# Performance work log

Hardware: AMD Instinct MI355X
Metric: run time of the kernel (lower is better)

The kernel has to match this reference:

```python
import jax, jax.numpy as jnp
import numpy as np

N_NODES = 100000
N_EDGES = 1600000
IN_DIM = 128      # 1 (degree) + 127 (raw feat)
HID = 128
N_GRAPHS = 100


def setup_inputs() -> dict:
    key = jax.random.key(0)
    ks = jax.random.split(key, 16)
    feat = jax.random.normal(ks[0], (N_NODES, IN_DIM - 1), dtype=jnp.float32)
    src = jax.random.randint(ks[1], (N_EDGES,), 0, N_NODES, dtype=jnp.int32)
    dst = jax.random.randint(ks[2], (N_EDGES,), 0, N_NODES, dtype=jnp.int32)
    graph_ids = jnp.sort(jax.random.randint(ks[3], (N_NODES,), 0, N_GRAPHS, dtype=jnp.int32))
    s = 1.0 / np.sqrt(IN_DIM)
    W0 = jax.random.uniform(ks[4], (HID, IN_DIM), jnp.float32, -s, s)
    b0 = jax.random.uniform(ks[5], (HID,), jnp.float32, -s, s)
    s = 1.0 / np.sqrt(HID)
    W1 = jax.random.uniform(ks[6], (HID, HID), jnp.float32, -s, s)
    b1 = jax.random.uniform(ks[7], (HID,), jnp.float32, -s, s)
    W2 = jax.random.uniform(ks[8], (HID, HID), jnp.float32, -s, s)
    b2 = jax.random.uniform(ks[9], (HID,), jnp.float32, -s, s)
    Wc1 = jax.random.uniform(ks[10], (HID, HID), jnp.float32, -s, s)
    bc1 = jax.random.uniform(ks[11], (HID,), jnp.float32, -s, s)
    Wc2 = jax.random.uniform(ks[12], (1, HID), jnp.float32, -s, s)
    bc2 = jax.random.uniform(ks[13], (1,), jnp.float32, -s, s)
    return {"feat": feat, "src": src, "dst": dst, "graph_ids": graph_ids,
            "num_graphs": N_GRAPHS,
            "W0": W0, "b0": b0, "W1": W1, "b1": b1, "W2": W2, "b2": b2,
            "Wc1": Wc1, "bc1": bc1, "Wc2": Wc2, "bc2": bc2}


def _gcn_layer(h, src, dst, deg, W, b):
    # mean over in-neighbor messages; zero-in-degree nodes keep old h (DGL reduce never fires)
    n = h.shape[0]
    summed = jax.ops.segment_sum(h[src], dst, num_segments=n)  # [N, d]
    mean = summed / jnp.maximum(deg, 1.0)[:, None]
    agg = jnp.where((deg > 0)[:, None], mean, h)
    return jax.nn.relu(agg @ W.T + b)


def reference(feat, src, dst, graph_ids, num_graphs,
              W0, b0, W1, b1, W2, b2, Wc1, bc1, Wc2, bc2):
    n = feat.shape[0]
    deg = jax.ops.segment_sum(jnp.ones(src.shape[0], jnp.float32), dst, num_segments=n)  # in-degrees
    h = jnp.concatenate([deg[:, None], feat], axis=-1)  # [N, IN_DIM]
    for W, b in ((W0, b0), (W1, b1), (W2, b2)):
        h = _gcn_layer(h, src, dst, deg, W, b)
    # dgl.mean_nodes: per-graph mean of node features
    counts = jax.ops.segment_sum(jnp.ones(n, jnp.float32), graph_ids, num_segments=num_graphs)
    hg = jax.ops.segment_sum(h, graph_ids, num_segments=num_graphs) / jnp.maximum(counts, 1.0)[:, None]
    # faithful: classify1 applied twice, no activation (F.relu was passed as bias flag)
    hg = hg @ Wc1.T + bc1
    hg = hg @ Wc1.T + bc1
    hg = hg @ Wc2.T + bc2
    return hg  # [num_graphs, 1]
```

## Files before the change

### kernel.cpp

```cpp
#include <hip/hip_runtime.h>
#include <hip/hip_bf16.h>

#define HID 128
#define NRAW 127
#define BSH 8
#define BNODES 256


typedef __attribute__((ext_vector_type(8))) short short8;
typedef __attribute__((ext_vector_type(4))) float floatx4;
typedef __attribute__((ext_vector_type(2))) float floatx2;

__device__ inline unsigned pack_bf2(float x, float y) {
    unsigned bx = __float_as_uint(x);
    unsigned by = __float_as_uint(y);
    bx += 0x7fffu + ((bx >> 16) & 1u);
    by += 0x7fffu + ((by >> 16) & 1u);
    return (bx >> 16) | (by & 0xffff0000u);
}
__device__ inline float bf_lo(unsigned u) { return __uint_as_float(u << 16); }
__device__ inline float bf_hi(unsigned u) { return __uint_as_float(u & 0xffff0000u); }


__global__ void init_kernel(const float* __restrict__ W0, const float* __restrict__ W1,
                            const float* __restrict__ W2, const float* __restrict__ Wc1,
                            unsigned* __restrict__ O0, unsigned* __restrict__ O1,
                            unsigned* __restrict__ O2, float* __restrict__ Wc1p,
                            int* __restrict__ gbucket, float* __restrict__ hg,
                            float* __restrict__ counts, int G) {
    int id = blockIdx.x * blockDim.x + threadIdx.x;
    if (id < 512) gbucket[id] = 0;
    if (id < G * HID) hg[id] = 0.f;
    if (id < G) counts[id] = 0.f;
    if (id < 16384) {
        int t = id >> 7, p = id & 127;
        Wc1p[id] = Wc1[t * 128 + ((p & 7) * 16 + (p >> 3))];
    }
    if (id < 3 * 8192) {
        int sel = id >> 13, l = id & 8191;
        const float* W = sel == 0 ? W0 : (sel == 1 ? W1 : W2);
        unsigned* O = sel == 0 ? O0 : (sel == 1 ? O1 : O2);
        int o = l >> 6, pp = (l & 63) * 2;
        int k0 = (pp & 7) * 16 + (pp >> 3);
        int k1 = ((pp + 1) & 7) * 16 + ((pp + 1) >> 3);
        O[l] = pack_bf2(W[o * 128 + k0], W[o * 128 + k1]);
    }
}


__global__ __launch_bounds__(256) void bucket_count_kernel(const int* __restrict__ dst,
                                                           int* __restrict__ gbucket,
                                                           int E, int NB) {
    __shared__ int hist[512];
    int t = threadIdx.x;
    for (int b = t; b < NB; b += 256) hist[b] = 0;
    __syncthreads();
    int base = blockIdx.x * 4096;
    #pragma unroll
    for (int j = 0; j < 16; ++j) {
        int e = base + j * 256 + t;
        if (e < E) atomicAdd(&hist[dst[e] >> BSH], 1);
    }
    __syncthreads();
    for (int b = t; b < NB; b += 256) {
        int v = hist[b];
        if (v) atomicAdd(&gbucket[b], v);
    }
}

__global__ void bucket_scan_kernel(const int* __restrict__ gbucket, int* __restrict__ bstart,
                                   int* __restrict__ gcur, int NB, int E) {
    __shared__ int sm[512];
    int t = threadIdx.x;
    int v = (t < NB) ? gbucket[t] : 0;
    sm[t] = v;
    __syncthreads();
    for (int off = 1; off < 512; off <<= 1) {
        int add = (t >= off) ? sm[t - off] : 0;
        __syncthreads();
        sm[t] += add;
        __syncthreads();
    }
    if (t < NB) {
        int ex = sm[t] - v;
        bstart[t] = ex;
        gcur[t] = ex;
    }
    if (t == 0) bstart[NB] = E;
}

__global__ __launch_bounds__(256) void bucket_scatter_kernel(const int* __restrict__ src,
                                                             const int* __restrict__ dst,
                                                             int* __restrict__ gcur,
                                                             uint2* __restrict__ staging,
                                                             int E, int NB) {
    __shared__ int hist[512];
    __shared__ int base[512];
    int t = threadIdx.x;
    for (int b = t; b < NB; b += 256) hist[b] = 0;
    __syncthreads();
    int s[16], d[16], r[16];
    int e0 = blockIdx.x * 4096;
    #pragma unroll
    for (int j = 0; j < 16; ++j) {
        int e = e0 + j * 256 + t;
        if (e < E) {
            s[j] = src[e];
            d[j] = dst[e];
            r[j] = atomicAdd(&hist[d[j] >> BSH], 1);
        } else d[j] = -1;
    }
    __syncthreads();
    for (int b = t; b < NB; b += 256) {
        int v = hist[b];
        base[b] = v ? atomicAdd(&gcur[b], v) : 0;
    }
    __syncthreads();
    #pragma unroll
    for (int j = 0; j < 16; ++j) {
        if (d[j] >= 0) {
            int b = d[j] >> BSH;
            staging[base[b] + r[j]] = make_uint2((unsigned)s[j], (unsigned)d[j]);
        }
    }
}

__global__ __launch_bounds__(256) void csr_build_kernel(const uint2* __restrict__ staging,
                                                        const int* __restrict__ bstart,
                                                        int* __restrict__ rp, int* __restrict__ csr,
                                                        float* __restrict__ degf,
                                                        int N, int E, int NB) {
    __shared__ int hist[256];
    __shared__ int sm[256];
    __shared__ int excl[256];
    __shared__ int cnt[256];
    int t = threadIdx.x;
    int b = blockIdx.x;
    int nbase = b << BSH;
    int s0 = bstart[b], e1 = bstart[b + 1];
    hist[t] = 0;
    __syncthreads();
    for (int i = s0 + t; i < e1; i += 256) {
        uint2 p = staging[i];
        atomicAdd(&hist[p.y & (BNODES - 1)], 1);
    }
    __syncthreads();
    int h = hist[t];
    sm[t] = h;
    __syncthreads();
    for (int off = 1; off < 256; off <<= 1) {
        int add = (t >= off) ? sm[t - off] : 0;
        __syncthreads();
        sm[t] += add;
        __syncthreads();
    }
    excl[t] = sm[t] - h;
    cnt[t] = 0;
    int n = nbase + t;
    if (n < N) {
        rp[n] = s0 + (sm[t] - h);
        degf[n] = (float)h;
    }
    if (b == NB - 1 && t == 0) rp[N] = E;
    __syncthreads();
    for (int i = s0 + t; i < e1; i += 256) {
        uint2 p = staging[i];
        int dl = p.y & (BNODES - 1);
        int pos = s0 + excl[dl] + atomicAdd(&cnt[dl], 1);
        csr[pos] = (int)p.x;
    }
}


__global__ void build_h0_kernel(const float* __restrict__ feat,
                                unsigned* __restrict__ h8, int N) {
    int id = blockIdx.x * blockDim.x + threadIdx.x;
    if (id >= N * 32) return;
    int n = id >> 5, c = id & 31;
    const float* fr = feat + (size_t)n * NRAW;
    int base = c >> 1, hb = (c & 1) * 4;
    float f[4];
    #pragma unroll
    for (int j = 0; j < 4; ++j) {
        int l = (hb + j) * 16 + base;
        f[j] = (l == 0) ? 0.f : fr[l - 1];
    }
    unsigned w = __builtin_amdgcn_cvt_pk_fp8_f32(f[0], f[1], 0, false);
    w = __builtin_amdgcn_cvt_pk_fp8_f32(f[2], f[3], w, true);
    h8[id] = w;
}


__global__ __launch_bounds__(256) void agg_fp8_kernel(const unsigned* __restrict__ h8,
                                                      unsigned* __restrict__ agg,
                                                      const int* __restrict__ rp,
                                                      const int* __restrict__ csr,
                                                      const float* __restrict__ degf, int N) {
    int t = threadIdx.x;
    int col = t & 15;
    int i = blockIdx.x * 16 + (t >> 4);
    if (i >= N) return;
    int start = rp[i], end = rp[i + 1];
    int deg = end - start;
    const uint2* h2 = (const uint2*)h8;
    if (deg == 0) {
        uint2 v = h2[(size_t)i * 16 + col];
        floatx2 l0 = __builtin_amdgcn_cvt_pk_f32_fp8(v.x, false);
        floatx2 h0 = __builtin_amdgcn_cvt_pk_f32_fp8(v.x, true);
        floatx2 l1 = __builtin_amdgcn_cvt_pk_f32_fp8(v.y, false);
        floatx2 h1 = __builtin_amdgcn_cvt_pk_f32_fp8(v.y, true);
        uint4 r;
        r.x = pack_bf2(l0[0], l0[1]);
        r.y = pack_bf2(h0[0], h0[1]);
        r.z = pack_bf2(l1[0], l1[1]);
        r.w = pack_bf2(h1[0], h1[1]);
        ((uint4*)agg)[(size_t)i * 16 + col] = r;
        return;
    }
    floatx2 a0 = {0.f, 0.f}, a1 = {0.f, 0.f}, a2 = {0.f, 0.f}, a3 = {0.f, 0.f};
    float dsum = 0.f;
    int p = start;
    for (; p + 4 <= end; p += 4) {
        int i0 = csr[p];
        int i1 = csr[p + 1];
        int i2 = csr[p + 2];
        int i3 = csr[p + 3];
        uint2 v0 = h2[(size_t)i0 * 16 + col];
        uint2 v1 = h2[(size_t)i1 * 16 + col];
        uint2 v2 = h2[(size_t)i2 * 16 + col];
        uint2 v3 = h2[(size_t)i3 * 16 + col];
        if (degf && col == 0) dsum += degf[i0] + degf[i1] + degf[i2] + degf[i3];
        a0 += __builtin_amdgcn_cvt_pk_f32_fp8(v0.x, false);
        a1 += __builtin_amdgcn_cvt_pk_f32_fp8(v0.x, true);
        a2 += __builtin_amdgcn_cvt_pk_f32_fp8(v0.y, false);
        a3 += __builtin_amdgcn_cvt_pk_f32_fp8(v0.y, true);
        a0 += __builtin_amdgcn_cvt_pk_f32_fp8(v1.x, false);
        a1 += __builtin_amdgcn_cvt_pk_f32_fp8(v1.x, true);
        a2 += __builtin_amdgcn_cvt_pk_f32_fp8(v1.y, false);
        a3 += __builtin_amdgcn_cvt_pk_f32_fp8(v1.y, true);
        a0 += __builtin_amdgcn_cvt_pk_f32_fp8(v2.x, false);
        a1 += __builtin_amdgcn_cvt_pk_f32_fp8(v2.x, true);
        a2 += __builtin_amdgcn_cvt_pk_f32_fp8(v2.y, false);
        a3 += __builtin_amdgcn_cvt_pk_f32_fp8(v2.y, true);
        a0 += __builtin_amdgcn_cvt_pk_f32_fp8(v3.x, false);
        a1 += __builtin_amdgcn_cvt_pk_f32_fp8(v3.x, true);
        a2 += __builtin_amdgcn_cvt_pk_f32_fp8(v3.y, false);
        a3 += __builtin_amdgcn_cvt_pk_f32_fp8(v3.y, true);
    }
    for (; p < end; ++p) {
        int i0 = csr[p];
        uint2 v0 = h2[(size_t)i0 * 16 + col];
        if (degf && col == 0) dsum += degf[i0];
        a0 += __builtin_amdgcn_cvt_pk_f32_fp8(v0.x, false);
        a1 += __builtin_amdgcn_cvt_pk_f32_fp8(v0.x, true);
        a2 += __builtin_amdgcn_cvt_pk_f32_fp8(v0.y, false);
        a3 += __builtin_amdgcn_cvt_pk_f32_fp8(v0.y, true);
    }
    if (degf && col == 0) a0[0] = dsum;
    float inv = 1.f / (float)deg;
    uint4 r;
    r.x = pack_bf2(a0[0] * inv, a0[1] * inv);
    r.y = pack_bf2(a1[0] * inv, a1[1] * inv);
    r.z = pack_bf2(a2[0] * inv, a2[1] * inv);
    r.w = pack_bf2(a3[0] * inv, a3[1] * inv);
    ((uint4*)agg)[(size_t)i * 16 + col] = r;
}


__global__ __launch_bounds__(256) void mfma_gemm_kernel(const unsigned* __restrict__ A,
                                                        unsigned* __restrict__ out8,
                                                        unsigned* __restrict__ outb,
                                                        const unsigned* __restrict__ Wb,
                                                        const float* __restrict__ bias, int N) {
    int t = threadIdx.x;
    int wv = t >> 6, lane = t & 63;
    int m = lane & 15, q = lane >> 4;
    int n0 = blockIdx.x * 64;
    const unsigned* abase = A + (size_t)(n0 + wv * 16 + m) * 64 + q * 4;

    floatx4 acc[8];
    #pragma unroll
    for (int ot = 0; ot < 8; ++ot) acc[ot] = (floatx4)(0.f);

    #pragma unroll
    for (int kt = 0; kt < 4; ++kt) {
        short8 af = *(const short8*)(abase + kt * 16);
        short8 bf[8];
        #pragma unroll
        for (int ot = 0; ot < 8; ++ot)
            bf[ot] = *(const short8*)&Wb[(ot * 16 + m) * 64 + kt * 16 + q * 4];
        #pragma unroll
        for (int ot = 0; ot < 8; ++ot)
            acc[ot] = __builtin_amdgcn_mfma_f32_16x16x32_bf16(af, bf[ot], acc[ot], 0, 0, 0);
    }

    float bv[8];
    #pragma unroll
    for (int ot = 0; ot < 8; ++ot) bv[ot] = bias[ot * 16 + m];

    #pragma unroll
    for (int r = 0; r < 4; ++r) {
        int n = n0 + wv * 16 + q * 4 + r;
        if (n < N) {
            float vv[8];
            #pragma unroll
            for (int ot = 0; ot < 8; ++ot) vv[ot] = fmaxf(acc[ot][r] + bv[ot], 0.f);
            if (out8) {
                unsigned w0 = __builtin_amdgcn_cvt_pk_fp8_f32(vv[0], vv[1], 0, false);
                w0 = __builtin_amdgcn_cvt_pk_fp8_f32(vv[2], vv[3], w0, true);
                unsigned w1 = __builtin_amdgcn_cvt_pk_fp8_f32(vv[4], vv[5], 0, false);
                w1 = __builtin_amdgcn_cvt_pk_fp8_f32(vv[6], vv[7], w1, true);
                ((uint2*)out8)[(size_t)n * 16 + m] = make_uint2(w0, w1);
            }
            if (outb) {
                uint4 w;
                w.x = pack_bf2(vv[0], vv[1]);
                w.y = pack_bf2(vv[2], vv[3]);
                w.z = pack_bf2(vv[4], vv[5]);
                w.w = pack_bf2(vv[6], vv[7]);
                ((uint4*)outb)[(size_t)n * 16 + m] = w;
            }
        }
    }
}


__global__ __launch_bounds__(256) void pool_kernel(const unsigned* __restrict__ h,
                                                   const int* __restrict__ gid,
                                                   float* __restrict__ hg,
                                                   float* __restrict__ counts, int N) {
    int c = threadIdx.x & 63;
    int q = threadIdx.x >> 6;
    int n0 = blockIdx.x * 64;
    int nend = min(n0 + 64, N);
    float ax = 0.f, ay = 0.f, cnt = 0.f;
    int cur = -1;
    for (int n = n0 + q; n < nend; n += 4) {
        int g = gid[n];
        if (g != cur) {
            if (cur >= 0) {
                atomicAdd(&hg[cur * HID + 2 * c], ax);
                atomicAdd(&hg[cur * HID + 2 * c + 1], ay);
                if (c == 0) atomicAdd(&counts[cur], cnt);
            }
            ax = ay = cnt = 0.f;
            cur = g;
        }
        unsigned v = h[(size_t)n * 64 + c];
        ax += bf_lo(v); ay += bf_hi(v);
        cnt += 1.f;
    }
    if (cur >= 0) {
        atomicAdd(&hg[cur * HID + 2 * c], ax);
        atomicAdd(&hg[cur * HID + 2 * c + 1], ay);
        if (c == 0) atomicAdd(&counts[cur], cnt);
    }
}


__global__ __launch_bounds__(128) void cls_fused_kernel(const float* __restrict__ hg,
                                                        const float* __restrict__ counts,
                                                        const float* __restrict__ Wc1p,
                                                        const float* __restrict__ Wc1,
                                                        const float* __restrict__ bc1,
                                                        const float* __restrict__ Wc2,
                                                        const float* __restrict__ bc2,
                                                        float* __restrict__ out, int G) {
    __shared__ float x[128];
    __shared__ float y[128];
    __shared__ float red[128];
    int g = blockIdx.x, t = threadIdx.x;
    float inv = 1.f / fmaxf(counts[g], 1.f);
    x[t] = hg[g * HID + t] * inv;
    __syncthreads();
    const float4* wp4 = (const float4*)(Wc1p + t * HID);
    float s = 0.f;
    #pragma unroll
    for (int k4 = 0; k4 < 32; ++k4) {
        float4 w = wp4[k4];
        s += x[k4 * 4] * w.x + x[k4 * 4 + 1] * w.y + x[k4 * 4 + 2] * w.z + x[k4 * 4 + 3] * w.w;
    }
    y[t] = s + bc1[t];
    __syncthreads();
    const float4* w4 = (const float4*)(Wc1 + t * HID);
    float s2 = 0.f;
    #pragma unroll
    for (int k4 = 0; k4 < 32; ++k4) {
        float4 w = w4[k4];
        s2 += y[k4 * 4] * w.x + y[k4 * 4 + 1] * w.y + y[k4 * 4 + 2] * w.z + y[k4 * 4 + 3] * w.w;
    }
    red[t] = (s2 + bc1[t]) * Wc2[t];
    __syncthreads();
    if (t < 64) {
        float r = red[t] + red[t + 64];
        #pragma unroll
        for (int off = 32; off > 0; off >>= 1) r += __shfl_down(r, off);
        if (t == 0) out[g] = r + bc2[0];
    }
}


extern "C" void kernel_launch(void* const* d_in, const int* in_sizes, int n_in,
                              void* d_out, int out_size, void* d_ws, size_t ws_size,
                              hipStream_t stream) {
    const float* feat = (const float*)d_in[0];
    const int* src    = (const int*)d_in[1];
    const int* dst    = (const int*)d_in[2];
    const int* gid    = (const int*)d_in[3];
    const float* W0  = (const float*)d_in[5];
    const float* b0  = (const float*)d_in[6];
    const float* W1  = (const float*)d_in[7];
    const float* b1  = (const float*)d_in[8];
    const float* W2  = (const float*)d_in[9];
    const float* b2  = (const float*)d_in[10];
    const float* Wc1 = (const float*)d_in[11];
    const float* bc1 = (const float*)d_in[12];
    const float* Wc2 = (const float*)d_in[13];
    const float* bc2 = (const float*)d_in[14];

    const int N = in_sizes[3];
    const int E = in_sizes[1];
    const int G = out_size;
    const int NB = (N + BNODES - 1) >> BSH;

    char* ws = (char*)d_ws;
    size_t off = 0;
    auto alloc = [&](size_t bytes) { void* p = ws + off; off += (bytes + 255) & ~size_t(255); return p; };
    unsigned* h8     = (unsigned*)alloc((size_t)N * 32 * 4);
    unsigned* hB     = (unsigned*)alloc((size_t)N * 64 * 4);
    unsigned* aggbuf = (unsigned*)alloc((size_t)N * 64 * 4);
    float* degf      = (float*)alloc((size_t)N * 4);
    uint2* staging   = (uint2*)alloc((size_t)E * 8);
    int* csr         = (int*)alloc((size_t)E * 4);
    int* rp          = (int*)alloc((size_t)(N + 1) * 4);
    int* gbucket     = (int*)alloc(512 * 4);
    int* bstart      = (int*)alloc(513 * 4);
    int* gcur        = (int*)alloc(512 * 4);
    unsigned* Wb0    = (unsigned*)alloc(8192 * 4);
    unsigned* Wb1    = (unsigned*)alloc(8192 * 4);
    unsigned* Wb2    = (unsigned*)alloc(8192 * 4);
    float* Wc1p      = (float*)alloc(16384 * 4);
    float* hg        = (float*)alloc((size_t)G * HID * 4);
    float* counts    = (float*)alloc((size_t)G * 4);

    init_kernel<<<96, 256, 0, stream>>>(W0, W1, W2, Wc1, Wb0, Wb1, Wb2, Wc1p,
                                        gbucket, hg, counts, G);

    int gE = (E + 4095) / 4096;
    bucket_count_kernel<<<gE, 256, 0, stream>>>(dst, gbucket, E, NB);
    bucket_scan_kernel<<<1, 512, 0, stream>>>(gbucket, bstart, gcur, NB, E);
    bucket_scatter_kernel<<<gE, 256, 0, stream>>>(src, dst, gcur, staging, E, NB);
    csr_build_kernel<<<NB, 256, 0, stream>>>(staging, bstart, rp, csr, degf, N, E, NB);

    build_h0_kernel<<<(N * 32 + 255) / 256, 256, 0, stream>>>(feat, h8, N);

    int agg_grid = (N + 15) / 16;
    int gemm_grid = (N + 63) / 64;

    agg_fp8_kernel<<<agg_grid, 256, 0, stream>>>(h8, aggbuf, rp, csr, degf, N);
    mfma_gemm_kernel<<<gemm_grid, 256, 0, stream>>>(aggbuf, h8, nullptr, Wb0, b0, N);

    agg_fp8_kernel<<<agg_grid, 256, 0, stream>>>(h8, aggbuf, rp, csr, nullptr, N);
    mfma_gemm_kernel<<<gemm_grid, 256, 0, stream>>>(aggbuf, h8, nullptr, Wb1, b1, N);

    agg_fp8_kernel<<<agg_grid, 256, 0, stream>>>(h8, aggbuf, rp, csr, nullptr, N);
    mfma_gemm_kernel<<<gemm_grid, 256, 0, stream>>>(aggbuf, nullptr, hB, Wb2, b2, N);

    pool_kernel<<<(N + 63) / 64, 256, 0, stream>>>(hB, gid, hg, counts, N);

    cls_fused_kernel<<<G, 128, 0, stream>>>(hg, counts, Wc1p, Wc1, bc1, Wc2, bc2,
                                            (float*)d_out, G);
}
```

Before: 426.9 us.

## Fuse neighbor aggregation and MFMA GEMM into one kernel per GCN layer

Each GCN layer becomes one kernel. It gathers and averages the fp8 neighbor features of 16 nodes into LDS as bf16, runs the 16x128x128 MFMA GEMM from LDS, then stages the outputs in LDS for coalesced global writes. This drops the bf16 aggregation buffer's global write and reread and three kernel launches. Because the old kernels read and wrote the same h8 buffer in turn, it also ping-pongs between two fp8 buffers so a layer never overwrites features it is still gathering. The cost is that each block now reloads the full weight matrix for only 16 nodes, and the LDS barriers may make the gather and GEMM phases wait on each other.

```diff
diff --git a/kernel.cpp b/kernel.cpp
--- a/kernel.cpp
+++ b/kernel.cpp
@@ -191,135 +191,124 @@
 }
 
 
-__global__ __launch_bounds__(256) void agg_fp8_kernel(const unsigned* __restrict__ h8,
-                                                      unsigned* __restrict__ agg,
-                                                      const int* __restrict__ rp,
-                                                      const int* __restrict__ csr,
-                                                      const float* __restrict__ degf, int N) {
-    int t = threadIdx.x;
-    int col = t & 15;
-    int i = blockIdx.x * 16 + (t >> 4);
-    if (i >= N) return;
-    int start = rp[i], end = rp[i + 1];
-    int deg = end - start;
-    const uint2* h2 = (const uint2*)h8;
-    if (deg == 0) {
-        uint2 v = h2[(size_t)i * 16 + col];
-        floatx2 l0 = __builtin_amdgcn_cvt_pk_f32_fp8(v.x, false);
-        floatx2 h0 = __builtin_amdgcn_cvt_pk_f32_fp8(v.x, true);
-        floatx2 l1 = __builtin_amdgcn_cvt_pk_f32_fp8(v.y, false);
-        floatx2 h1 = __builtin_amdgcn_cvt_pk_f32_fp8(v.y, true);
-        uint4 r;
-        r.x = pack_bf2(l0[0], l0[1]);
-        r.y = pack_bf2(h0[0], h0[1]);
-        r.z = pack_bf2(l1[0], l1[1]);
-        r.w = pack_bf2(h1[0], h1[1]);
-        ((uint4*)agg)[(size_t)i * 16 + col] = r;
-        return;
-    }
-    floatx2 a0 = {0.f, 0.f}, a1 = {0.f, 0.f}, a2 = {0.f, 0.f}, a3 = {0.f, 0.f};
-    float dsum = 0.f;
-    int p = start;
-    for (; p + 4 <= end; p += 4) {
-        int i0 = csr[p];
-        int i1 = csr[p + 1];
-        int i2 = csr[p + 2];
-        int i3 = csr[p + 3];
-        uint2 v0 = h2[(size_t)i0 * 16 + col];
-        uint2 v1 = h2[(size_t)i1 * 16 + col];
-        uint2 v2 = h2[(size_t)i2 * 16 + col];
-        uint2 v3 = h2[(size_t)i3 * 16 + col];
-        if (degf && col == 0) dsum += degf[i0] + degf[i1] + degf[i2] + degf[i3];
-        a0 += __builtin_amdgcn_cvt_pk_f32_fp8(v0.x, false);
-        a1 += __builtin_amdgcn_cvt_pk_f32_fp8(v0.x, true);
-        a2 += __builtin_amdgcn_cvt_pk_f32_fp8(v0.y, false);
-        a3 += __builtin_amdgcn_cvt_pk_f32_fp8(v0.y, true);
-        a0 += __builtin_amdgcn_cvt_pk_f32_fp8(v1.x, false);
-        a1 += __builtin_amdgcn_cvt_pk_f32_fp8(v1.x, true);
-        a2 += __builtin_amdgcn_cvt_pk_f32_fp8(v1.y, false);
-        a3 += __builtin_amdgcn_cvt_pk_f32_fp8(v1.y, true);
-        a0 += __builtin_amdgcn_cvt_pk_f32_fp8(v2.x, false);
-        a1 += __builtin_amdgcn_cvt_pk_f32_fp8(v2.x, true);
-        a2 += __builtin_amdgcn_cvt_pk_f32_fp8(v2.y, false);
-        a3 += __builtin_amdgcn_cvt_pk_f32_fp8(v2.y, true);
-        a0 += __builtin_amdgcn_cvt_pk_f32_fp8(v3.x, false);
-        a1 += __builtin_amdgcn_cvt_pk_f32_fp8(v3.x, true);
-        a2 += __builtin_amdgcn_cvt_pk_f32_fp8(v3.y, false);
-        a3 += __builtin_amdgcn_cvt_pk_f32_fp8(v3.y, true);
-    }
-    for (; p < end; ++p) {
-        int i0 = csr[p];
-        uint2 v0 = h2[(size_t)i0 * 16 + col];
-        if (degf && col == 0) dsum += degf[i0];
-        a0 += __builtin_amdgcn_cvt_pk_f32_fp8(v0.x, false);
-        a1 += __builtin_amdgcn_cvt_pk_f32_fp8(v0.x, true);
-        a2 += __builtin_amdgcn_cvt_pk_f32_fp8(v0.y, false);
-        a3 += __builtin_amdgcn_cvt_pk_f32_fp8(v0.y, true);
-    }
-    if (degf && col == 0) a0[0] = dsum;
-    float inv = 1.f / (float)deg;
-    uint4 r;
-    r.x = pack_bf2(a0[0] * inv, a0[1] * inv);
-    r.y = pack_bf2(a1[0] * inv, a1[1] * inv);
-    r.z = pack_bf2(a2[0] * inv, a2[1] * inv);
-    r.w = pack_bf2(a3[0] * inv, a3[1] * inv);
-    ((uint4*)agg)[(size_t)i * 16 + col] = r;
-}
-
-
-__global__ __launch_bounds__(256) void mfma_gemm_kernel(const unsigned* __restrict__ A,
+__global__ __launch_bounds__(256) void gcn_fused_kernel(const unsigned* __restrict__ h8,
                                                         unsigned* __restrict__ out8,
                                                         unsigned* __restrict__ outb,
                                                         const unsigned* __restrict__ Wb,
-                                                        const float* __restrict__ bias, int N) {
+                                                        const float* __restrict__ bias,
+                                                        const int* __restrict__ rp,
+                                                        const int* __restrict__ csr,
+                                                        const float* __restrict__ degf, int N) {
+    __shared__ unsigned Al[16 * 64];
+    __shared__ unsigned Cs[16 * 64];
     int t = threadIdx.x;
+    int col = t & 15;
+    int g = t >> 4;
+    int n0 = blockIdx.x * 16;
+    int i = n0 + g;
+    const uint2* h2 = (const uint2*)h8;
+
+    if (i < N) {
+        int start = rp[i], end = rp[i + 1];
+        int deg = end - start;
+        uint4 r;
+        if (deg == 0) {
+            uint2 v = h2[(size_t)i * 16 + col];
+            floatx2 l0 = __builtin_amdgcn_cvt_pk_f32_fp8(v.x, false);
+            floatx2 h0 = __builtin_amdgcn_cvt_pk_f32_fp8(v.x, true);
+            floatx2 l1 = __builtin_amdgcn_cvt_pk_f32_fp8(v.y, false);
+            floatx2 h1 = __builtin_amdgcn_cvt_pk_f32_fp8(v.y, true);
+            r.x = pack_bf2(l0[0], l0[1]);
+            r.y = pack_bf2(h0[0], h0[1]);
+            r.z = pack_bf2(l1[0], l1[1]);
+            r.w = pack_bf2(h1[0], h1[1]);
+        } else {
+            floatx2 a0 = {0.f, 0.f}, a1 = {0.f, 0.f}, a2 = {0.f, 0.f}, a3 = {0.f, 0.f};
+            float dsum = 0.f;
+            int p = start;
+            for (; p + 4 <= end; p += 4) {
+                int i0 = csr[p];
+                int i1 = csr[p + 1];
+                int i2 = csr[p + 2];
+                int i3 = csr[p + 3];
+                uint2 v0 = h2[(size_t)i0 * 16 + col];
+                uint2 v1 = h2[(size_t)i1 * 16 + col];
+                uint2 v2 = h2[(size_t)i2 * 16 + col];
+                uint2 v3 = h2[(size_t)i3 * 16 + col];
+                if (degf && col == 0) dsum += degf[i0] + degf[i1] + degf[i2] + degf[i3];
+                a0 += __builtin_amdgcn_cvt_pk_f32_fp8(v0.x, false);
+                a1 += __builtin_amdgcn_cvt_pk_f32_fp8(v0.x, true);
+                a2 += __builtin_amdgcn_cvt_pk_f32_fp8(v0.y, false);
+                a3 += __builtin_amdgcn_cvt_pk_f32_fp8(v0.y, true);
+                a0 += __builtin_amdgcn_cvt_pk_f32_fp8(v1.x, false);
+                a1 += __builtin_amdgcn_cvt_pk_f32_fp8(v1.x, true);
+                a2 += __builtin_amdgcn_cvt_pk_f32_fp8(v1.y, false);
+                a3 += __builtin_amdgcn_cvt_pk_f32_fp8(v1.y, true);
+                a0 += __builtin_amdgcn_cvt_pk_f32_fp8(v2.x, false);
+                a1 += __builtin_amdgcn_cvt_pk_f32_fp8(v2.x, true);
+                a2 += __builtin_amdgcn_cvt_pk_f32_fp8(v2.y, false);
+                a3 += __builtin_amdgcn_cvt_pk_f32_fp8(v2.y, true);
+                a0 += __builtin_amdgcn_cvt_pk_f32_fp8(v3.x, false);
+                a1 += __builtin_amdgcn_cvt_pk_f32_fp8(v3.x, true);
+                a2 += __builtin_amdgcn_cvt_pk_f32_fp8(v3.y, false);
+                a3 += __builtin_amdgcn_cvt_pk_f32_fp8(v3.y, true);
+            }
+            for (; p < end; ++p) {
+                int i0 = csr[p];
+                uint2 v0 = h2[(size_t)i0 * 16 + col];
+                if (degf && col == 0) dsum += degf[i0];
+                a0 += __builtin_amdgcn_cvt_pk_f32_fp8(v0.x, false);
+                a1 += __builtin_amdgcn_cvt_pk_f32_fp8(v0.x, true);
+                a2 += __builtin_amdgcn_cvt_pk_f32_fp8(v0.y, false);
+                a3 += __builtin_amdgcn_cvt_pk_f32_fp8(v0.y, true);
+            }
+            if (degf && col == 0) a0[0] = dsum;
+            float inv = 1.f / (float)deg;
+            r.x = pack_bf2(a0[0] * inv, a0[1] * inv);
+            r.y = pack_bf2(a1[0] * inv, a1[1] * inv);
+            r.z = pack_bf2(a2[0] * inv, a2[1] * inv);
+            r.w = pack_bf2(a3[0] * inv, a3[1] * inv);
+        }
+        *(uint4*)&Al[(g * 16 + col) * 4] = r;
+    }
+    __syncthreads();
+
     int wv = t >> 6, lane = t & 63;
     int m = lane & 15, q = lane >> 4;
-    int n0 = blockIdx.x * 64;
-    const unsigned* abase = A + (size_t)(n0 + wv * 16 + m) * 64 + q * 4;
-
-    floatx4 acc[8];
-    #pragma unroll
-    for (int ot = 0; ot < 8; ++ot) acc[ot] = (floatx4)(0.f);
-
+    floatx4 acc0 = (floatx4)(0.f), acc1 = (floatx4)(0.f);
     #pragma unroll
     for (int kt = 0; kt < 4; ++kt) {
-        short8 af = *(const short8*)(abase + kt * 16);
-        short8 bf[8];
-        #pragma unroll
-        for (int ot = 0; ot < 8; ++ot)
-            bf[ot] = *(const short8*)&Wb[(ot * 16 + m) * 64 + kt * 16 + q * 4];
-        #pragma unroll
-        for (int ot = 0; ot < 8; ++ot)
-            acc[ot] = __builtin_amdgcn_mfma_f32_16x16x32_bf16(af, bf[ot], acc[ot], 0, 0, 0);
-    }
-
-    float bv[8];
-    #pragma unroll
-    for (int ot = 0; ot < 8; ++ot) bv[ot] = bias[ot * 16 + m];
-
-    #pragma unroll
-    for (int r = 0; r < 4; ++r) {
-        int n = n0 + wv * 16 + q * 4 + r;
+        short8 af = *(const short8*)&Al[m * 64 + (kt * 4 + q) * 4];
+        short8 b0 = *(const short8*)&Wb[((2 * wv) * 16 + m) * 64 + kt * 16 + q * 4];
+        short8 b1 = *(const short8*)&Wb[((2 * wv + 1) * 16 + m) * 64 + kt * 16 + q * 4];
+        acc0 = __builtin_amdgcn_mfma_f32_16x16x32_bf16(af, b0, acc0, 0, 0, 0);
+        acc1 = __builtin_amdgcn_mfma_f32_16x16x32_bf16(af, b1, acc1, 0, 0, 0);
+    }
+    float bv0 = bias[(2 * wv) * 16 + m];
+    float bv1 = bias[(2 * wv + 1) * 16 + m];
+    #pragma unroll
+    for (int r4 = 0; r4 < 4; ++r4) {
+        int row = q * 4 + r4;
+        float v0 = fmaxf(acc0[r4] + bv0, 0.f);
+        float v1 = fmaxf(acc1[r4] + bv1, 0.f);
+        if (out8) {
+            unsigned pk = __builtin_amdgcn_cvt_pk_fp8_f32(v0, v1, 0, false);
+            *(unsigned short*)((char*)Cs + row * 128 + m * 8 + 2 * wv) = (unsigned short)pk;
+        } else {
+            Cs[row * 64 + m * 4 + wv] = pack_bf2(v0, v1);
+        }
+    }
+    __syncthreads();
+
+    {
+        int row = t >> 4, c = t & 15;
+        int n = n0 + row;
         if (n < N) {
-            float vv[8];
-            #pragma unroll
-            for (int ot = 0; ot < 8; ++ot) vv[ot] = fmaxf(acc[ot][r] + bv[ot], 0.f);
-            if (out8) {
-                unsigned w0 = __builtin_amdgcn_cvt_pk_fp8_f32(vv[0], vv[1], 0, false);
-                w0 = __builtin_amdgcn_cvt_pk_fp8_f32(vv[2], vv[3], w0, true);
-                unsigned w1 = __builtin_amdgcn_cvt_pk_fp8_f32(vv[4], vv[5], 0, false);
-                w1 = __builtin_amdgcn_cvt_pk_fp8_f32(vv[6], vv[7], w1, true);
-                ((uint2*)out8)[(size_t)n * 16 + m] = make_uint2(w0, w1);
-            }
-            if (outb) {
-                uint4 w;
-                w.x = pack_bf2(vv[0], vv[1]);
-                w.y = pack_bf2(vv[2], vv[3]);
-                w.z = pack_bf2(vv[4], vv[5]);
-                w.w = pack_bf2(vv[6], vv[7]);
-                ((uint4*)outb)[(size_t)n * 16 + m] = w;
-            }
+            if (out8)
+                ((uint2*)out8)[(size_t)n * 16 + c] =
+                    *(const uint2*)((const char*)Cs + row * 128 + c * 8);
+            else
+                ((uint4*)outb)[(size_t)n * 16 + c] = *(const uint4*)&Cs[row * 64 + c * 4];
         }
     }
 }
@@ -426,9 +415,9 @@
     char* ws = (char*)d_ws;
     size_t off = 0;
     auto alloc = [&](size_t bytes) { void* p = ws + off; off += (bytes + 255) & ~size_t(255); return p; };
-    unsigned* h8     = (unsigned*)alloc((size_t)N * 32 * 4);
+    unsigned* h8a    = (unsigned*)alloc((size_t)N * 32 * 4);
+    unsigned* h8b    = (unsigned*)alloc((size_t)N * 32 * 4);
     unsigned* hB     = (unsigned*)alloc((size_t)N * 64 * 4);
-    unsigned* aggbuf = (unsigned*)alloc((size_t)N * 64 * 4);
     float* degf      = (float*)alloc((size_t)N * 4);
     uint2* staging   = (uint2*)alloc((size_t)E * 8);
     int* csr         = (int*)alloc((size_t)E * 4);
@@ -452,19 +441,12 @@
     bucket_scatter_kernel<<<gE, 256, 0, stream>>>(src, dst, gcur, staging, E, NB);
     csr_build_kernel<<<NB, 256, 0, stream>>>(staging, bstart, rp, csr, degf, N, E, NB);
 
-    build_h0_kernel<<<(N * 32 + 255) / 256, 256, 0, stream>>>(feat, h8, N);
-
-    int agg_grid = (N + 15) / 16;
-    int gemm_grid = (N + 63) / 64;
-
-    agg_fp8_kernel<<<agg_grid, 256, 0, stream>>>(h8, aggbuf, rp, csr, degf, N);
-    mfma_gemm_kernel<<<gemm_grid, 256, 0, stream>>>(aggbuf, h8, nullptr, Wb0, b0, N);
-
-    agg_fp8_kernel<<<agg_grid, 256, 0, stream>>>(h8, aggbuf, rp, csr, nullptr, N);
-    mfma_gemm_kernel<<<gemm_grid, 256, 0, stream>>>(aggbuf, h8, nullptr, Wb1, b1, N);
-
-    agg_fp8_kernel<<<agg_grid, 256, 0, stream>>>(h8, aggbuf, rp, csr, nullptr, N);
-    mfma_gemm_kernel<<<gemm_grid, 256, 0, stream>>>(aggbuf, nullptr, hB, Wb2, b2, N);
+    build_h0_kernel<<<(N * 32 + 255) / 256, 256, 0, stream>>>(feat, h8a, N);
+
+    int layer_grid = (N + 15) / 16;
+    gcn_fused_kernel<<<layer_grid, 256, 0, stream>>>(h8a, h8b, nullptr, Wb0, b0, rp, csr, degf, N);
+    gcn_fused_kernel<<<layer_grid, 256, 0, stream>>>(h8b, h8a, nullptr, Wb1, b1, rp, csr, nullptr, N);
+    gcn_fused_kernel<<<layer_grid, 256, 0, stream>>>(h8a, nullptr, hB, Wb2, b2, rp, csr, nullptr, N);
 
     pool_kernel<<<(N + 63) / 64, 256, 0, stream>>>(hB, gid, hg, counts, N);
 
```

New measurement: 382.6 us. 10.4% less time.
